# Kernel optimization log

Measured on AMD Instinct MI355X. Metric: run time of the kernel, lower is better.

The kernel has to match this reference:

```python
import jax, jax.numpy as jnp
import numpy as np

B, S, H, NH = 32, 512, 768, 12
EC, EU = 4, 4
CAP = 1.0
DH = H // NH
CAPACITY = int(CAP * B / EC)  # Switch-style capacity per common expert


def setup_inputs() -> dict:
    key = jax.random.key(0)
    ks = jax.random.split(key, 10)
    s = 0.02
    E = EC + EU  # experts stacked: [0:EC]=common, [EC:]=unique
    return {
        "hidden_states": jax.random.normal(ks[0], (B, S, H), jnp.float32),
        "attention_mask": jnp.zeros((B, S), jnp.float32),  # additive mask
        "Wq": jax.random.normal(ks[1], (E, H, H), jnp.float32) * s,
        "bq": jnp.zeros((E, H), jnp.float32),
        "Wk": jax.random.normal(ks[2], (E, H, H), jnp.float32) * s,
        "bk": jnp.zeros((E, H), jnp.float32),
        "Wv": jax.random.normal(ks[3], (E, H, H), jnp.float32) * s,
        "bv": jnp.zeros((E, H), jnp.float32),
        "Wo": jax.random.normal(ks[4], (E, H, H), jnp.float32) * s,
        "bo": jnp.zeros((E, H), jnp.float32),
        "Wsc": jax.random.normal(ks[5], (H, EC), jnp.float32) * s,
        "bsc": jnp.zeros((EC,), jnp.float32),
        "Wsu": jax.random.normal(ks[6], (H, EU), jnp.float32) * s,
        "bsu": jnp.zeros((EU,), jnp.float32),
    }


def reference(hidden_states, attention_mask, Wq, bq, Wk, bk, Wv, bv, Wo, bo,
              Wsc, bsc, Wsu, bsu):
    # ---- common routing (per-sequence top-1 over mean-pooled tokens) ----
    h_mean = hidden_states.mean(axis=1)                       # [B,H]
    pc = jax.nn.softmax(h_mean @ Wsc + bsc, axis=-1)          # [B,EC]
    rc = jnp.argmax(pc, axis=-1)                              # [B]
    pc_max = jnp.max(pc, axis=-1)                             # [B]
    # capacity drop: within each expert keep the CAPACITY highest-prob seqs
    order = jnp.argsort(-pc_max)                              # global desc sort
    oh = jax.nn.one_hot(rc[order], EC, dtype=jnp.int32)       # [B,EC]
    rank = jnp.take_along_axis(jnp.cumsum(oh, axis=0), rc[order][:, None], 1)[:, 0]
    kept = jnp.zeros((B,), bool).at[order].set(rank <= CAPACITY)

    # ---- unique routing for dropped sequences (mean is per-sequence, so
    #      computing on the full batch and masking matches torch) ----
    pu = jax.nn.softmax(h_mean @ Wsu + bsu, axis=-1)          # [B,EU]
    ru = jnp.argmax(pu, axis=-1)
    pu_max = jnp.max(pu, axis=-1)

    # per-sequence expert index into stacked [EC+EU] expert params
    eidx = jnp.where(kept, rc, EC + ru)                       # [B]
    # scaling factor p/stop_grad(p): ==1 in fwd, routes grads to the gate
    scale = jnp.where(kept,
                      pc_max / jax.lax.stop_gradient(pc_max),
                      pu_max / jax.lax.stop_gradient(pu_max))

    # ---- gather-dispatch: per-sequence expert weights ----
    Wq_b, Wk_b, Wv_b, Wo_b = Wq[eidx], Wk[eidx], Wv[eidx], Wo[eidx]  # [B,H,H]
    bq_b, bk_b, bv_b, bo_b = bq[eidx], bk[eidx], bv[eidx], bo[eidx]  # [B,H]

    def heads(t):  # [B,S,H] -> [B,NH,S,DH]
        return t.reshape(B, S, NH, DH).transpose(0, 2, 1, 3)

    q = heads(jnp.einsum('bsh,bhd->bsd', hidden_states, Wq_b) + bq_b[:, None, :])
    k = heads(jnp.einsum('bsh,bhd->bsd', hidden_states, Wk_b) + bk_b[:, None, :])
    v = heads(jnp.einsum('bsh,bhd->bsd', hidden_states, Wv_b) + bv_b[:, None, :])

    scores = jnp.einsum('bhsd,bhtd->bhst', q, k) / np.float32(np.sqrt(DH))
    scores = scores + attention_mask[:, None, None, :]        # additive mask
    attn = jax.nn.softmax(scores, axis=-1)
    ctx = jnp.einsum('bhst,bhtd->bhsd', attn, v)
    ctx = ctx.transpose(0, 2, 1, 3).reshape(B, S, H)

    out = jnp.einsum('bsh,bhd->bsd', ctx, Wo_b) + bo_b[:, None, :]
    return out * scale[:, None, None]
```

## Files before the change

kernel.cpp:

```cpp
#include <hip/hip_runtime.h>
#include <hip/hip_bf16.h>

#define B_ 32
#define S_ 512
#define H_ 768
#define NH_ 12
#define DH_ 64
#define EC_ 4
#define CAPN_ 8

using short8  = __attribute__((ext_vector_type(8))) short;
using floatx4 = __attribute__((ext_vector_type(4))) float;
using bf16 = __hip_bfloat16;

__device__ __forceinline__ void gl_lds16(const void* g, void* l) {
  __builtin_amdgcn_global_load_lds(
      (const __attribute__((address_space(1))) unsigned int*)g,
      (__attribute__((address_space(3))) unsigned int*)l, 16, 0, 0);
}

__global__ void k_mean_convert(const float* __restrict__ X, bf16* __restrict__ Xh,
                               float* __restrict__ partial) {
  int idx = blockIdx.x * 256 + threadIdx.x;
  int b = idx / H_, h = idx - b * H_;
  int s0 = blockIdx.y * 64;
  size_t base = ((size_t)b * S_ + s0) * H_ + h;
  float sum = 0.f;
#pragma unroll 8
  for (int s = 0; s < 64; ++s) {
    float v = X[base + (size_t)s * H_];
    Xh[base + (size_t)s * H_] = __float2bfloat16(v);
    sum += v;
  }
  partial[(size_t)blockIdx.y * (B_ * H_) + idx] = sum;
}

__global__ void k_mean_reduce(const float* __restrict__ partial, float* __restrict__ hmean) {
  int idx = blockIdx.x * 256 + threadIdx.x;
  float s = 0.f;
#pragma unroll
  for (int c = 0; c < 8; ++c) s += partial[(size_t)c * (B_ * H_) + idx];
  hmean[idx] = s * (1.f / 512.f);
}

__global__ void k_wt(const float* __restrict__ Wq, const float* __restrict__ Wk,
                     const float* __restrict__ Wv, const float* __restrict__ Wo,
                     bf16* __restrict__ Wt) {
  __shared__ float tile[32][33];
  int z = blockIdx.z;
  const float* Wbase = (z < 8 ? Wq : z < 16 ? Wk : z < 24 ? Wv : Wo) + (size_t)(z & 7) * H_ * H_;
  int k0 = blockIdx.x * 32, n0 = blockIdx.y * 32;
  int tj = threadIdx.x & 31, ti = threadIdx.x >> 5;
#pragma unroll
  for (int r = 0; r < 4; ++r)
    tile[ti + r * 8][tj] = Wbase[(size_t)(k0 + ti + r * 8) * H_ + n0 + tj];
  __syncthreads();
  bf16* out = Wt + (size_t)z * H_ * H_;
#pragma unroll
  for (int r = 0; r < 4; ++r)
    out[(size_t)(n0 + ti + r * 8) * H_ + k0 + tj] = __float2bfloat16(tile[tj][ti + r * 8]);
}

__global__ void k_route(const float* __restrict__ hmean,
                        const float* __restrict__ Wsc, const float* __restrict__ bsc,
                        const float* __restrict__ Wsu, const float* __restrict__ bsu,
                        int* __restrict__ eidx) {
  __shared__ float logit[B_][8];
  __shared__ float pcmax[B_];
  __shared__ int rc_s[B_], ru_s[B_];
  int t = threadIdx.x;
  {
    int b = t >> 3, g = t & 7;
    const float* w = (g < 4) ? (Wsc + g) : (Wsu + (g - 4));
    float acc = (g < 4) ? bsc[g] : bsu[g - 4];
    const float* hm = hmean + (size_t)b * H_;
    for (int hh = 0; hh < H_; ++hh) acc += hm[hh] * w[hh * 4];
    logit[b][g] = acc;
  }
  __syncthreads();
  if (t < B_) {
    float m = logit[t][0]; int a = 0;
    for (int e = 1; e < 4; ++e) if (logit[t][e] > m) { m = logit[t][e]; a = e; }
    float s = 0.f;
    for (int e = 0; e < 4; ++e) s += expf(logit[t][e] - m);
    pcmax[t] = 1.f / s;
    rc_s[t] = a;
    float mu = logit[t][4]; int au = 0;
    for (int e = 1; e < 4; ++e) if (logit[t][4 + e] > mu) { mu = logit[t][4 + e]; au = e; }
    ru_s[t] = au;
  }
  __syncthreads();
  if (t == 0) {
    bool used[B_], kept[B_];
    int cnt[EC_] = {0, 0, 0, 0};
    for (int i = 0; i < B_; ++i) used[i] = false;
    for (int i = 0; i < B_; ++i) {
      int best = 0; float bv = -1e30f;
      for (int j = 0; j < B_; ++j)
        if (!used[j] && pcmax[j] > bv) { bv = pcmax[j]; best = j; }
      used[best] = true;
      kept[best] = (++cnt[rc_s[best]] <= CAPN_);
    }
    for (int i = 0; i < B_; ++i)
      eidx[i] = kept[i] ? rc_s[i] : EC_ + ru_s[i];
  }
}

template <int OMODE>
__global__ __launch_bounds__(256) void k_gemm(
    const bf16* __restrict__ A, const bf16* __restrict__ Wt,
    const float* __restrict__ bias0, const float* __restrict__ bias1,
    const float* __restrict__ bias2,
    void* out0, void* out1, void* out2,
    const int* __restrict__ eidx, int mat0) {
  __shared__ __align__(16) char lds[32768];
  int bz = blockIdx.z;
  int b = blockIdx.y;
  int e = eidx[b];
  int mtile = blockIdx.x & 3, ntile = blockIdx.x >> 2;
  int m0 = mtile * 128, n0 = ntile * 128;
  const bf16* Ab = A + (size_t)b * S_ * H_;
  const bf16* Wb = Wt + (size_t)((mat0 + bz) * 8 + e) * H_ * H_;
  const float* bias = ((bz == 0) ? bias0 : (bz == 1) ? bias1 : bias2) + (size_t)e * H_;
  void* outp = (bz == 0) ? out0 : (bz == 1) ? out1 : out2;

  int t = threadIdx.x, lane = t & 63, w = t >> 6;
  int wm = (w & 1) * 64, wn = (w >> 1) * 64;
  int lm = lane & 15, lq = lane >> 4;

  floatx4 acc[4][4] = {};
  for (int kt = 0; kt < 12; ++kt) {
    __syncthreads();
#pragma unroll
    for (int r = 0; r < 8; ++r) {
      int c = t + r * 256;
      const bf16* g;
      if (c < 1024) {
        int mm = c >> 3, pos = c & 7, kc = pos ^ (mm & 7);
        g = Ab + (size_t)(m0 + mm) * H_ + kt * 64 + kc * 8;
      } else {
        int c2 = c - 1024;
        int nn = c2 >> 3, pos = c2 & 7, kc = pos ^ (nn & 7);
        g = Wb + (size_t)(n0 + nn) * H_ + kt * 64 + kc * 8;
      }
      gl_lds16(g, lds + (size_t)c * 16);
    }
    __syncthreads();
#pragma unroll
    for (int kf = 0; kf < 2; ++kf) {
      int kc = kf * 4 + lq;
      short8 af[4], bf[4];
#pragma unroll
      for (int mf = 0; mf < 4; ++mf) {
        int mm = wm + mf * 16 + lm;
        af[mf] = *(const short8*)(lds + ((size_t)(mm * 8 + (kc ^ (mm & 7)))) * 16);
      }
#pragma unroll
      for (int nf = 0; nf < 4; ++nf) {
        int nn = wn + nf * 16 + lm;
        bf[nf] = *(const short8*)(lds + 16384 + ((size_t)(nn * 8 + (kc ^ (nn & 7)))) * 16);
      }
#pragma unroll
      for (int mf = 0; mf < 4; ++mf)
#pragma unroll
        for (int nf = 0; nf < 4; ++nf)
          acc[mf][nf] = __builtin_amdgcn_mfma_f32_16x16x32_bf16(af[mf], bf[nf], acc[mf][nf], 0, 0, 0);
    }
  }
#pragma unroll
  for (int mf = 0; mf < 4; ++mf) {
#pragma unroll
    for (int nf = 0; nf < 4; ++nf) {
      int n = n0 + wn + nf * 16 + lm;
      float bv = bias[n];
      int mrow = m0 + wm + mf * 16 + lq * 4;
      size_t rowbase = ((size_t)b * S_ + mrow) * H_ + n;
#pragma unroll
      for (int r = 0; r < 4; ++r) {
        float v = acc[mf][nf][r] + bv;
        if (OMODE == 0) {
          if (bz == 2) {
            int s = mrow + r;
            ((bf16*)outp)[((size_t)(b * NH_ + (n >> 6))) * 32768 +
                          (size_t)(s >> 3) * 512 + (n & 63) * 8 + (s & 7)] =
                __float2bfloat16(v);
          } else {
            ((bf16*)outp)[rowbase + (size_t)r * H_] = __float2bfloat16(v);
          }
        } else {
          ((float*)outp)[rowbase + (size_t)r * H_] = v;
        }
      }
    }
  }
}

__global__ __launch_bounds__(256, 3) void k_attn(
    const bf16* __restrict__ Q, const bf16* __restrict__ K,
    const bf16* __restrict__ Vt, const float* __restrict__ mask,
    bf16* __restrict__ Ctx) {
  __shared__ __align__(16) char bufA[8192];
  __shared__ __align__(16) char bufB[8192];
  __shared__ __align__(16) bf16 sc[32 * 520];
  __shared__ float redmax[4][32];
  __shared__ float redsum[4][32];

  int qt = blockIdx.x, h = blockIdx.y, b = blockIdx.z;
  int q0 = qt * 32;
  int t = threadIdx.x, lane = t & 63, w = t >> 6;
  int lm = lane & 15, lq = lane >> 4;

  short8 qf[2][2];
#pragma unroll
  for (int mf = 0; mf < 2; ++mf)
#pragma unroll
    for (int kf = 0; kf < 2; ++kf)
      qf[mf][kf] = *(const short8*)(Q + ((size_t)(b * S_ + q0 + mf * 16 + lm)) * H_ +
                                    h * DH_ + kf * 32 + lq * 8);
  float mv[8];
#pragma unroll
  for (int kt = 0; kt < 8; ++kt)
    mv[kt] = mask[(size_t)b * S_ + kt * 64 + w * 16 + lm];

  {
#pragma unroll
    for (int r = 0; r < 2; ++r) {
      int c = t + r * 256, s = c >> 3, pos = c & 7, kc = pos ^ (s & 7);
      gl_lds16(K + ((size_t)(b * S_ + s)) * H_ + h * DH_ + kc * 8, bufA + (size_t)c * 16);
    }
  }
  floatx4 acc[8][2] = {};
  for (int kt = 0; kt < 8; ++kt) {
    __syncthreads();
    if (kt < 7) {
      char* nb = ((kt + 1) & 1) ? bufB : bufA;
#pragma unroll
      for (int r = 0; r < 2; ++r) {
        int c = t + r * 256, s = c >> 3, pos = c & 7, kc = pos ^ (s & 7);
        gl_lds16(K + ((size_t)(b * S_ + (kt + 1) * 64 + s)) * H_ + h * DH_ + kc * 8,
                 nb + (size_t)c * 16);
      }
    }
    const char* kb = (kt & 1) ? bufB : bufA;
#pragma unroll
    for (int kf = 0; kf < 2; ++kf) {
      int row = w * 16 + lm, kc = kf * 4 + lq;
      short8 bfr = *(const short8*)(kb + ((size_t)(row * 8 + (kc ^ (row & 7)))) * 16);
#pragma unroll
      for (int mf = 0; mf < 2; ++mf)
        acc[kt][mf] = __builtin_amdgcn_mfma_f32_16x16x32_bf16(qf[mf][kf], bfr, acc[kt][mf], 0, 0, 0);
    }
  }
  __syncthreads();

  const bf16* vbase = Vt + ((size_t)(b * NH_ + h)) * 64 * 512;
  {
#pragma unroll
    for (int r = 0; r < 2; ++r) {
      int c = t + r * 256;
      gl_lds16(vbase + (size_t)c * 8, bufA + (size_t)c * 16);
    }
  }

  float rmax[2][4];
#pragma unroll
  for (int mf = 0; mf < 2; ++mf)
#pragma unroll
    for (int r = 0; r < 4; ++r) rmax[mf][r] = -1e30f;
#pragma unroll
  for (int kt = 0; kt < 8; ++kt)
#pragma unroll
    for (int mf = 0; mf < 2; ++mf)
#pragma unroll
      for (int r = 0; r < 4; ++r) {
        float s = acc[kt][mf][r] * 0.125f + mv[kt];
        acc[kt][mf][r] = s;
        rmax[mf][r] = fmaxf(rmax[mf][r], s);
      }
#pragma unroll
  for (int st = 1; st < 16; st <<= 1)
#pragma unroll
    for (int mf = 0; mf < 2; ++mf)
#pragma unroll
      for (int r = 0; r < 4; ++r)
        rmax[mf][r] = fmaxf(rmax[mf][r], __shfl_xor(rmax[mf][r], st, 64));
  if (lm == 0) {
#pragma unroll
    for (int mf = 0; mf < 2; ++mf)
#pragma unroll
      for (int r = 0; r < 4; ++r) redmax[w][mf * 16 + lq * 4 + r] = rmax[mf][r];
  }
  __syncthreads();
#pragma unroll
  for (int mf = 0; mf < 2; ++mf)
#pragma unroll
    for (int r = 0; r < 4; ++r) {
      int row = mf * 16 + lq * 4 + r;
      rmax[mf][r] = fmaxf(fmaxf(redmax[0][row], redmax[1][row]),
                          fmaxf(redmax[2][row], redmax[3][row]));
    }
  float rsum[2][4] = {};
#pragma unroll
  for (int kt = 0; kt < 8; ++kt) {
    int col = kt * 64 + w * 16 + lm;
#pragma unroll
    for (int mf = 0; mf < 2; ++mf)
#pragma unroll
      for (int r = 0; r < 4; ++r) {
        float e = __expf(acc[kt][mf][r] - rmax[mf][r]);
        rsum[mf][r] += e;
        sc[(mf * 16 + lq * 4 + r) * 520 + col] = __float2bfloat16(e);
      }
  }
#pragma unroll
  for (int st = 1; st < 16; st <<= 1)
#pragma unroll
    for (int mf = 0; mf < 2; ++mf)
#pragma unroll
      for (int r = 0; r < 4; ++r)
        rsum[mf][r] += __shfl_xor(rsum[mf][r], st, 64);
  if (lm == 0) {
#pragma unroll
    for (int mf = 0; mf < 2; ++mf)
#pragma unroll
      for (int r = 0; r < 4; ++r) redsum[w][mf * 16 + lq * 4 + r] = rsum[mf][r];
  }
  __syncthreads();
  float inv[2][4];
#pragma unroll
  for (int mf = 0; mf < 2; ++mf)
#pragma unroll
    for (int r = 0; r < 4; ++r) {
      int row = mf * 16 + lq * 4 + r;
      inv[mf][r] = 1.f / (redsum[0][row] + redsum[1][row] + redsum[2][row] + redsum[3][row]);
    }

  floatx4 oacc[2] = {};
  for (int kt = 0; kt < 8; ++kt) {
    if (kt) __syncthreads();
    if (kt < 7) {
      char* nb = ((kt + 1) & 1) ? bufB : bufA;
#pragma unroll
      for (int r = 0; r < 2; ++r) {
        int c = t + r * 256;
        gl_lds16(vbase + ((size_t)((kt + 1) * 512 + c)) * 8, nb + (size_t)c * 16);
      }
    }
    const char* vb = (kt & 1) ? bufB : bufA;
#pragma unroll
    for (int kf = 0; kf < 2; ++kf) {
      int dh = w * 16 + lm;
      short8 bfr = *(const short8*)(vb + ((size_t)((kf * 4 + lq) * 64 + dh)) * 16);
#pragma unroll
      for (int mf = 0; mf < 2; ++mf) {
        int row = mf * 16 + lm;
        short8 af = *(const short8*)((const char*)sc +
                        ((size_t)(row * 520 + kt * 64 + kf * 32 + lq * 8)) * 2);
        oacc[mf] = __builtin_amdgcn_mfma_f32_16x16x32_bf16(af, bfr, oacc[mf], 0, 0, 0);
      }
    }
  }
  int dh = w * 16 + lm;
#pragma unroll
  for (int mf = 0; mf < 2; ++mf)
#pragma unroll
    for (int r = 0; r < 4; ++r) {
      int row = mf * 16 + lq * 4 + r;
      Ctx[((size_t)(b * S_ + q0 + row)) * H_ + h * DH_ + dh] =
          __float2bfloat16(oacc[mf][r] * inv[mf][r]);
    }
}

extern "C" void kernel_launch(void* const* d_in, const int* in_sizes, int n_in,
                              void* d_out, int out_size, void* d_ws, size_t ws_size,
                              hipStream_t stream) {
  const float* X    = (const float*)d_in[0];
  const float* mask = (const float*)d_in[1];
  const float* Wq   = (const float*)d_in[2];
  const float* bq   = (const float*)d_in[3];
  const float* Wk   = (const float*)d_in[4];
  const float* bk   = (const float*)d_in[5];
  const float* Wv   = (const float*)d_in[6];
  const float* bv   = (const float*)d_in[7];
  const float* Wo   = (const float*)d_in[8];
  const float* bo   = (const float*)d_in[9];
  const float* Wsc  = (const float*)d_in[10];
  const float* bsc  = (const float*)d_in[11];
  const float* Wsu  = (const float*)d_in[12];
  const float* bsu  = (const float*)d_in[13];

  char* ws = (char*)d_ws;
  int*   eidx    = (int*)ws;
  float* partial = (float*)(ws + 256);
  float* hmean   = (float*)(ws + 786688);
  bf16*  Xh      = (bf16*)(ws + 884992);
  bf16*  Wt      = (bf16*)(ws + 26050816);
  bf16*  qb      = (bf16*)(ws + 63799552);
  bf16*  kb      = (bf16*)(ws + 88965376);
  bf16*  Vt      = (bf16*)(ws + 139297024);
  bf16*  ctx     = Xh;

  k_mean_convert<<<dim3(96, 8), 256, 0, stream>>>(X, Xh, partial);
  k_mean_reduce<<<96, 256, 0, stream>>>(partial, hmean);
  k_wt<<<dim3(24, 24, 32), 256, 0, stream>>>(Wq, Wk, Wv, Wo, Wt);
  k_route<<<1, 256, 0, stream>>>(hmean, Wsc, bsc, Wsu, bsu, eidx);
  k_gemm<0><<<dim3(24, 32, 3), 256, 0, stream>>>(Xh, Wt, bq, bk, bv,
                                                 (void*)qb, (void*)kb, (void*)Vt, eidx, 0);
  k_attn<<<dim3(16, NH_, B_), 256, 0, stream>>>(qb, kb, Vt, mask, ctx);
  k_gemm<1><<<dim3(24, 32, 1), 256, 0, stream>>>(ctx, Wt, bo, bo, bo,
                                                 d_out, d_out, d_out, eidx, 3);
}
```

Baseline: 498.7 us.

## Rewrite attention as per-wave online-softmax and parallelize gate logits

Attention is restructured so each wave owns 32 query rows and streams K and V tiles straight from global memory. It keeps a running max and sum (online softmax) and stages only a small per-wave P tile in LDS, so block-wide barriers, the full score buffer and the cross-wave reductions go away. The grid shrinks to 4 query blocks per head, and K/V fragments are loaded directly instead of through async LDS double-buffering. The single-block routing kernel is also split into a 32-block gate-logit kernel with shuffle reductions plus a small routing kernel, which shortens a serial step on the critical path. The trade-off is that K/V are no longer shared across waves through LDS, so global and L2 traffic per block rises.

```diff
diff --git a/kernel.cpp b/kernel.cpp
--- a/kernel.cpp
+++ b/kernel.cpp
@@ -61,32 +61,42 @@
     out[(size_t)(n0 + ti + r * 8) * H_ + k0 + tj] = __float2bfloat16(tile[tj][ti + r * 8]);
 }
 
-__global__ void k_route(const float* __restrict__ hmean,
-                        const float* __restrict__ Wsc, const float* __restrict__ bsc,
-                        const float* __restrict__ Wsu, const float* __restrict__ bsu,
-                        int* __restrict__ eidx) {
-  __shared__ float logit[B_][8];
+__global__ void k_gate(const float* __restrict__ hmean,
+                       const float* __restrict__ Wsc, const float* __restrict__ bsc,
+                       const float* __restrict__ Wsu, const float* __restrict__ bsu,
+                       float* __restrict__ logits) {
+  int b = blockIdx.x;
+  int t = threadIdx.x;
+  int g = t >> 3, p = t & 7;
+  const float* hm = hmean + (size_t)b * H_;
+  const float* w;
+  float bias;
+  if (g < 4) { w = Wsc + g; bias = bsc[g]; }
+  else       { w = Wsu + (g - 4); bias = bsu[g - 4]; }
+  float acc = 0.f;
+  for (int j = p; j < H_; j += 8) acc += hm[j] * w[j * 4];
+  acc += __shfl_xor(acc, 1);
+  acc += __shfl_xor(acc, 2);
+  acc += __shfl_xor(acc, 4);
+  if (p == 0) logits[b * 8 + g] = acc + bias;
+}
+
+__global__ void k_route2(const float* __restrict__ logits, int* __restrict__ eidx) {
   __shared__ float pcmax[B_];
   __shared__ int rc_s[B_], ru_s[B_];
   int t = threadIdx.x;
-  {
-    int b = t >> 3, g = t & 7;
-    const float* w = (g < 4) ? (Wsc + g) : (Wsu + (g - 4));
-    float acc = (g < 4) ? bsc[g] : bsu[g - 4];
-    const float* hm = hmean + (size_t)b * H_;
-    for (int hh = 0; hh < H_; ++hh) acc += hm[hh] * w[hh * 4];
-    logit[b][g] = acc;
-  }
-  __syncthreads();
   if (t < B_) {
-    float m = logit[t][0]; int a = 0;
-    for (int e = 1; e < 4; ++e) if (logit[t][e] > m) { m = logit[t][e]; a = e; }
+    float lg[8];
+#pragma unroll
+    for (int e = 0; e < 8; ++e) lg[e] = logits[t * 8 + e];
+    float m = lg[0]; int a = 0;
+    for (int e = 1; e < 4; ++e) if (lg[e] > m) { m = lg[e]; a = e; }
     float s = 0.f;
-    for (int e = 0; e < 4; ++e) s += expf(logit[t][e] - m);
+    for (int e = 0; e < 4; ++e) s += expf(lg[e] - m);
     pcmax[t] = 1.f / s;
     rc_s[t] = a;
-    float mu = logit[t][4]; int au = 0;
-    for (int e = 1; e < 4; ++e) if (logit[t][4 + e] > mu) { mu = logit[t][4 + e]; au = e; }
+    float mu = lg[4]; int au = 0;
+    for (int e = 1; e < 4; ++e) if (lg[4 + e] > mu) { mu = lg[4 + e]; au = e; }
     ru_s[t] = au;
   }
   __syncthreads();
@@ -199,16 +209,12 @@
     const bf16* __restrict__ Q, const bf16* __restrict__ K,
     const bf16* __restrict__ Vt, const float* __restrict__ mask,
     bf16* __restrict__ Ctx) {
-  __shared__ __align__(16) char bufA[8192];
-  __shared__ __align__(16) char bufB[8192];
-  __shared__ __align__(16) bf16 sc[32 * 520];
-  __shared__ float redmax[4][32];
-  __shared__ float redsum[4][32];
-
-  int qt = blockIdx.x, h = blockIdx.y, b = blockIdx.z;
-  int q0 = qt * 32;
+  __shared__ __align__(16) bf16 ldsP[4][32 * 72];
+
+  int h = blockIdx.y, b = blockIdx.z;
   int t = threadIdx.x, lane = t & 63, w = t >> 6;
   int lm = lane & 15, lq = lane >> 4;
+  int q0 = blockIdx.x * 128 + w * 32;
 
   short8 qf[2][2];
 #pragma unroll
@@ -217,158 +223,102 @@
     for (int kf = 0; kf < 2; ++kf)
       qf[mf][kf] = *(const short8*)(Q + ((size_t)(b * S_ + q0 + mf * 16 + lm)) * H_ +
                                     h * DH_ + kf * 32 + lq * 8);
-  float mv[8];
-#pragma unroll
-  for (int kt = 0; kt < 8; ++kt)
-    mv[kt] = mask[(size_t)b * S_ + kt * 64 + w * 16 + lm];
-
-  {
-#pragma unroll
-    for (int r = 0; r < 2; ++r) {
-      int c = t + r * 256, s = c >> 3, pos = c & 7, kc = pos ^ (s & 7);
-      gl_lds16(K + ((size_t)(b * S_ + s)) * H_ + h * DH_ + kc * 8, bufA + (size_t)c * 16);
-    }
-  }
-  floatx4 acc[8][2] = {};
+
+  const bf16* vtb = Vt + ((size_t)(b * NH_ + h)) * 32768;
+  bf16* myP = ldsP[w];
+
+  floatx4 oacc[2][4] = {};
+  float m_[2][4], l_[2][4];
+#pragma unroll
+  for (int mf = 0; mf < 2; ++mf)
+#pragma unroll
+    for (int r = 0; r < 4; ++r) { m_[mf][r] = -1e30f; l_[mf][r] = 0.f; }
+
   for (int kt = 0; kt < 8; ++kt) {
-    __syncthreads();
-    if (kt < 7) {
-      char* nb = ((kt + 1) & 1) ? bufB : bufA;
-#pragma unroll
-      for (int r = 0; r < 2; ++r) {
-        int c = t + r * 256, s = c >> 3, pos = c & 7, kc = pos ^ (s & 7);
-        gl_lds16(K + ((size_t)(b * S_ + (kt + 1) * 64 + s)) * H_ + h * DH_ + kc * 8,
-                 nb + (size_t)c * 16);
-      }
-    }
-    const char* kb = (kt & 1) ? bufB : bufA;
+    floatx4 s[2][4] = {};
+    float mv4[4];
+#pragma unroll
+    for (int nf = 0; nf < 4; ++nf)
+      mv4[nf] = mask[(size_t)b * S_ + kt * 64 + nf * 16 + lm];
 #pragma unroll
     for (int kf = 0; kf < 2; ++kf) {
-      int row = w * 16 + lm, kc = kf * 4 + lq;
-      short8 bfr = *(const short8*)(kb + ((size_t)(row * 8 + (kc ^ (row & 7)))) * 16);
+      short8 kb4[4];
+#pragma unroll
+      for (int nf = 0; nf < 4; ++nf)
+        kb4[nf] = *(const short8*)(K + ((size_t)(b * S_ + kt * 64 + nf * 16 + lm)) * H_ +
+                                   h * DH_ + kf * 32 + lq * 8);
 #pragma unroll
       for (int mf = 0; mf < 2; ++mf)
-        acc[kt][mf] = __builtin_amdgcn_mfma_f32_16x16x32_bf16(qf[mf][kf], bfr, acc[kt][mf], 0, 0, 0);
-    }
-  }
-  __syncthreads();
-
-  const bf16* vbase = Vt + ((size_t)(b * NH_ + h)) * 64 * 512;
-  {
-#pragma unroll
-    for (int r = 0; r < 2; ++r) {
-      int c = t + r * 256;
-      gl_lds16(vbase + (size_t)c * 8, bufA + (size_t)c * 16);
-    }
-  }
-
-  float rmax[2][4];
-#pragma unroll
-  for (int mf = 0; mf < 2; ++mf)
-#pragma unroll
-    for (int r = 0; r < 4; ++r) rmax[mf][r] = -1e30f;
-#pragma unroll
-  for (int kt = 0; kt < 8; ++kt)
-#pragma unroll
-    for (int mf = 0; mf < 2; ++mf)
+#pragma unroll
+        for (int nf = 0; nf < 4; ++nf)
+          s[mf][nf] = __builtin_amdgcn_mfma_f32_16x16x32_bf16(qf[mf][kf], kb4[nf], s[mf][nf], 0, 0, 0);
+    }
+#pragma unroll
+    for (int mf = 0; mf < 2; ++mf) {
 #pragma unroll
       for (int r = 0; r < 4; ++r) {
-        float s = acc[kt][mf][r] * 0.125f + mv[kt];
-        acc[kt][mf][r] = s;
-        rmax[mf][r] = fmaxf(rmax[mf][r], s);
-      }
-#pragma unroll
-  for (int st = 1; st < 16; st <<= 1)
-#pragma unroll
-    for (int mf = 0; mf < 2; ++mf)
-#pragma unroll
-      for (int r = 0; r < 4; ++r)
-        rmax[mf][r] = fmaxf(rmax[mf][r], __shfl_xor(rmax[mf][r], st, 64));
-  if (lm == 0) {
-#pragma unroll
-    for (int mf = 0; mf < 2; ++mf)
-#pragma unroll
-      for (int r = 0; r < 4; ++r) redmax[w][mf * 16 + lq * 4 + r] = rmax[mf][r];
-  }
-  __syncthreads();
-#pragma unroll
-  for (int mf = 0; mf < 2; ++mf)
-#pragma unroll
-    for (int r = 0; r < 4; ++r) {
-      int row = mf * 16 + lq * 4 + r;
-      rmax[mf][r] = fmaxf(fmaxf(redmax[0][row], redmax[1][row]),
-                          fmaxf(redmax[2][row], redmax[3][row]));
-    }
-  float rsum[2][4] = {};
-#pragma unroll
-  for (int kt = 0; kt < 8; ++kt) {
-    int col = kt * 64 + w * 16 + lm;
-#pragma unroll
-    for (int mf = 0; mf < 2; ++mf)
-#pragma unroll
-      for (int r = 0; r < 4; ++r) {
-        float e = __expf(acc[kt][mf][r] - rmax[mf][r]);
-        rsum[mf][r] += e;
-        sc[(mf * 16 + lq * 4 + r) * 520 + col] = __float2bfloat16(e);
-      }
-  }
-#pragma unroll
-  for (int st = 1; st < 16; st <<= 1)
-#pragma unroll
-    for (int mf = 0; mf < 2; ++mf)
-#pragma unroll
-      for (int r = 0; r < 4; ++r)
-        rsum[mf][r] += __shfl_xor(rsum[mf][r], st, 64);
-  if (lm == 0) {
-#pragma unroll
-    for (int mf = 0; mf < 2; ++mf)
-#pragma unroll
-      for (int r = 0; r < 4; ++r) redsum[w][mf * 16 + lq * 4 + r] = rsum[mf][r];
-  }
-  __syncthreads();
-  float inv[2][4];
-#pragma unroll
-  for (int mf = 0; mf < 2; ++mf)
-#pragma unroll
-    for (int r = 0; r < 4; ++r) {
-      int row = mf * 16 + lq * 4 + r;
-      inv[mf][r] = 1.f / (redsum[0][row] + redsum[1][row] + redsum[2][row] + redsum[3][row]);
-    }
-
-  floatx4 oacc[2] = {};
-  for (int kt = 0; kt < 8; ++kt) {
-    if (kt) __syncthreads();
-    if (kt < 7) {
-      char* nb = ((kt + 1) & 1) ? bufB : bufA;
-#pragma unroll
-      for (int r = 0; r < 2; ++r) {
-        int c = t + r * 256;
-        gl_lds16(vbase + ((size_t)((kt + 1) * 512 + c)) * 8, nb + (size_t)c * 16);
-      }
-    }
-    const char* vb = (kt & 1) ? bufB : bufA;
+#pragma unroll
+        for (int nf = 0; nf < 4; ++nf)
+          s[mf][nf][r] = s[mf][nf][r] * 0.125f + mv4[nf];
+        float tm = fmaxf(fmaxf(s[mf][0][r], s[mf][1][r]), fmaxf(s[mf][2][r], s[mf][3][r]));
+        tm = fmaxf(tm, __shfl_xor(tm, 1));
+        tm = fmaxf(tm, __shfl_xor(tm, 2));
+        tm = fmaxf(tm, __shfl_xor(tm, 4));
+        tm = fmaxf(tm, __shfl_xor(tm, 8));
+        float mn = fmaxf(m_[mf][r], tm);
+        float a = __expf(m_[mf][r] - mn);
+        m_[mf][r] = mn;
+        int row = mf * 16 + lq * 4 + r;
+        float ps = 0.f;
+#pragma unroll
+        for (int nf = 0; nf < 4; ++nf) {
+          float p = __expf(s[mf][nf][r] - mn);
+          ps += p;
+          int col = (nf * 16 + lm) ^ (lq << 3);
+          myP[row * 72 + col] = __float2bfloat16(p);
+        }
+        ps += __shfl_xor(ps, 1);
+        ps += __shfl_xor(ps, 2);
+        ps += __shfl_xor(ps, 4);
+        ps += __shfl_xor(ps, 8);
+        l_[mf][r] = l_[mf][r] * a + ps;
+#pragma unroll
+        for (int nf = 0; nf < 4; ++nf) oacc[mf][nf][r] *= a;
+      }
+    }
 #pragma unroll
     for (int kf = 0; kf < 2; ++kf) {
-      int dh = w * 16 + lm;
-      short8 bfr = *(const short8*)(vb + ((size_t)((kf * 4 + lq) * 64 + dh)) * 16);
+      short8 pf[2];
 #pragma unroll
       for (int mf = 0; mf < 2; ++mf) {
         int row = mf * 16 + lm;
-        short8 af = *(const short8*)((const char*)sc +
-                        ((size_t)(row * 520 + kt * 64 + kf * 32 + lq * 8)) * 2);
-        oacc[mf] = __builtin_amdgcn_mfma_f32_16x16x32_bf16(af, bfr, oacc[mf], 0, 0, 0);
-      }
-    }
-  }
-  int dh = w * 16 + lm;
-#pragma unroll
-  for (int mf = 0; mf < 2; ++mf)
+        int ksw = (kf * 32 + lq * 8) ^ ((((row >> 2) & 3)) << 3);
+        pf[mf] = *(const short8*)&myP[row * 72 + ksw];
+      }
+      short8 vf4[4];
+#pragma unroll
+      for (int nf = 0; nf < 4; ++nf)
+        vf4[nf] = *(const short8*)(vtb + ((size_t)(kt * 8 + kf * 4 + lq)) * 512 +
+                                   (nf * 16 + lm) * 8);
+#pragma unroll
+      for (int mf = 0; mf < 2; ++mf)
+#pragma unroll
+        for (int nf = 0; nf < 4; ++nf)
+          oacc[mf][nf] = __builtin_amdgcn_mfma_f32_16x16x32_bf16(pf[mf], vf4[nf], oacc[mf][nf], 0, 0, 0);
+    }
+  }
+#pragma unroll
+  for (int mf = 0; mf < 2; ++mf) {
 #pragma unroll
     for (int r = 0; r < 4; ++r) {
-      int row = mf * 16 + lq * 4 + r;
-      Ctx[((size_t)(b * S_ + q0 + row)) * H_ + h * DH_ + dh] =
-          __float2bfloat16(oacc[mf][r] * inv[mf][r]);
-    }
+      float inv = 1.f / l_[mf][r];
+      int row = q0 + mf * 16 + lq * 4 + r;
+#pragma unroll
+      for (int nf = 0; nf < 4; ++nf)
+        Ctx[((size_t)(b * S_ + row)) * H_ + h * DH_ + nf * 16 + lm] =
+            __float2bfloat16(oacc[mf][nf][r] * inv);
+    }
+  }
 }
 
 extern "C" void kernel_launch(void* const* d_in, const int* in_sizes, int n_in,
@@ -391,22 +341,24 @@
 
   char* ws = (char*)d_ws;
   int*   eidx    = (int*)ws;
-  float* partial = (float*)(ws + 256);
-  float* hmean   = (float*)(ws + 786688);
-  bf16*  Xh      = (bf16*)(ws + 884992);
-  bf16*  Wt      = (bf16*)(ws + 26050816);
-  bf16*  qb      = (bf16*)(ws + 63799552);
-  bf16*  kb      = (bf16*)(ws + 88965376);
-  bf16*  Vt      = (bf16*)(ws + 139297024);
+  float* logits  = (float*)(ws + 128);
+  float* partial = (float*)(ws + 1280);
+  float* hmean   = (float*)(ws + 787712);
+  bf16*  Xh      = (bf16*)(ws + 886016);
+  bf16*  Wt      = (bf16*)(ws + 26051840);
+  bf16*  qb      = (bf16*)(ws + 63800576);
+  bf16*  kb      = (bf16*)(ws + 88966400);
+  bf16*  Vt      = (bf16*)(ws + 114132224);
   bf16*  ctx     = Xh;
 
   k_mean_convert<<<dim3(96, 8), 256, 0, stream>>>(X, Xh, partial);
   k_mean_reduce<<<96, 256, 0, stream>>>(partial, hmean);
   k_wt<<<dim3(24, 24, 32), 256, 0, stream>>>(Wq, Wk, Wv, Wo, Wt);
-  k_route<<<1, 256, 0, stream>>>(hmean, Wsc, bsc, Wsu, bsu, eidx);
+  k_gate<<<B_, 64, 0, stream>>>(hmean, Wsc, bsc, Wsu, bsu, logits);
+  k_route2<<<1, 64, 0, stream>>>(logits, eidx);
   k_gemm<0><<<dim3(24, 32, 3), 256, 0, stream>>>(Xh, Wt, bq, bk, bv,
                                                  (void*)qb, (void*)kb, (void*)Vt, eidx, 0);
-  k_attn<<<dim3(16, NH_, B_), 256, 0, stream>>>(qb, kb, Vt, mask, ctx);
+  k_attn<<<dim3(4, NH_, B_), 256, 0, stream>>>(qb, kb, Vt, mask, ctx);
   k_gemm<1><<<dim3(24, 32, 1), 256, 0, stream>>>(ctx, Wt, bo, bo, bo,
                                                  d_out, d_out, d_out, eidx, 3);
 }
```

New measurement: 506.5 us. No clear change (+1.6%).
